# Kernel optimization log

Hardware: AMD Instinct MI355X
Metric: run time of the kernel (lower is better)

## Reference

```python
import jax, jax.numpy as jnp
import numpy as np


def setup_inputs() -> dict:
    key = jax.random.key(0)
    k1, k2 = jax.random.split(key)
    B, S, F = 8, 2048, 128
    feature = jax.random.normal(k1, (B, S, F), dtype=jnp.float32)
    noise = jax.random.normal(k2, (B, S, S), dtype=jnp.float32)
    return {"feature": feature, "noise": noise}


def reference(feature, noise):
    # stability: inverse variance over feat dim (torch.var is unbiased -> ddof=1)
    var = jnp.var(feature, axis=2, ddof=1, keepdims=True)          # [B, S, 1]
    stability = 1.0 / (var + 1e-6)
    stability = stability / jnp.max(stability)                      # global max normalize
    # scale per-row noise and softmax over keys (last dim)
    scaled = noise * stability                                      # [B, S, S]
    path = jax.nn.softmax(scaled, axis=-1)                          # [B, S, S]
    # weighted sum of frames
    return jnp.einsum('bij,bjf->bif', path, feature)                # [B, S, F]
```

## Files before the change

### kernel.cpp

```cpp
#include <hip/hip_runtime.h>
#include <hip/hip_bf16.h>

#define BATCH 8
#define SEQ   2048
#define FEATD 128
#define IBLK  32
#define JT    64
#define KSPLIT 2
#define KLEN  (SEQ / KSPLIT)
#define NJT   (KLEN / JT)

typedef __attribute__((ext_vector_type(8))) short short8;
typedef __attribute__((ext_vector_type(4))) float f32x4;

__device__ __forceinline__ unsigned short f2bf(float f) {
  unsigned int u = __float_as_uint(f);
  u += 0x7fffu + ((u >> 16) & 1u);
  return (unsigned short)(u >> 16);
}

__device__ __forceinline__ void gll16(const unsigned short* gsrc, unsigned short* lds) {
  __builtin_amdgcn_global_load_lds(
      (const __attribute__((address_space(1))) void*)gsrc,
      (__attribute__((address_space(3))) void*)lds, 16, 0, 0);
}

__global__ __launch_bounds__(256)
void prep_kernel(const float* __restrict__ feature,
                 float* __restrict__ stab,
                 unsigned int* __restrict__ gmax,
                 unsigned short* __restrict__ featT) {
  __shared__ float tile[32][133];
  __shared__ float wmax[4];
  int bid = blockIdx.x;
  int b   = bid >> 6;
  int j0  = (bid & 63) * 32;
  int t   = threadIdx.x;
  int r   = t >> 3;
  int seg = t & 7;

  const float* rp = feature + ((size_t)(b * SEQ + j0 + r)) * FEATD + seg * 16;
  float s = 0.0f, ss = 0.0f;
  #pragma unroll
  for (int k = 0; k < 4; k++) {
    float4 v = ((const float4*)rp)[k];
    tile[r][seg * 16 + k * 4 + 0] = v.x;
    tile[r][seg * 16 + k * 4 + 1] = v.y;
    tile[r][seg * 16 + k * 4 + 2] = v.z;
    tile[r][seg * 16 + k * 4 + 3] = v.w;
    s  += v.x + v.y + v.z + v.w;
    ss += v.x * v.x + v.y * v.y + v.z * v.z + v.w * v.w;
  }
  #pragma unroll
  for (int d = 1; d < 8; d <<= 1) {
    s  += __shfl_xor(s, d, 8);
    ss += __shfl_xor(ss, d, 8);
  }
  float st = 0.0f;
  if (seg == 0) {
    float var = (ss - s * s * (1.0f / 128.0f)) * (1.0f / 127.0f);
    st = 1.0f / (var + 1e-6f);
    stab[(size_t)b * SEQ + j0 + r] = st;
  }
  float m = st;
  #pragma unroll
  for (int d = 1; d < 64; d <<= 1) m = fmaxf(m, __shfl_xor(m, d, 64));
  if ((t & 63) == 0) wmax[t >> 6] = m;
  __syncthreads();
  if (t == 0) {
    float mm = fmaxf(fmaxf(wmax[0], wmax[1]), fmaxf(wmax[2], wmax[3]));
    atomicMax(gmax, __float_as_uint(mm));
  }
  int f  = t >> 1;
  int jh = t & 1;
  unsigned short obuf[16];
  #pragma unroll
  for (int jj = 0; jj < 16; jj++) obuf[jj] = f2bf(tile[jh * 16 + jj][f]);
  unsigned short* dst = featT + ((size_t)(b * FEATD + f)) * SEQ + j0 + jh * 16;
  *(uint4*)(dst)     = *(const uint4*)&obuf[0];
  *(uint4*)(dst + 8) = *(const uint4*)&obuf[8];
}

#define LOADN4(JTV, N0, N1, N2, N3) { \
    const float4* p_ = (const float4*)(nbase + (size_t)(JTV) * JT); \
    N0 = p_[0]; N1 = p_[1]; N2 = p_[8]; N3 = p_[9]; }

#define PROCB(N0, N1, N2, N3, PK0, PK1) { \
    float x_[16] = {N0.x, N0.y, N0.z, N0.w, N1.x, N1.y, N1.z, N1.w, \
                    N2.x, N2.y, N2.z, N2.w, N3.x, N3.y, N3.z, N3.w}; \
    _Pragma("unroll") \
    for (int k_ = 0; k_ < 8; k_++) { \
      float e_ = __expf(x_[k_] * sn); psum += e_; PK0[k_] = (short)f2bf(e_); } \
    _Pragma("unroll") \
    for (int k_ = 0; k_ < 8; k_++) { \
      float e_ = __expf(x_[8 + k_] * sn); psum += e_; PK1[k_] = (short)f2bf(e_); } }

#define GLLSLOT(JTV, SLOT) { \
    gll16(g0 + (size_t)(JTV) * JT, l0 + (SLOT) * (FEATD * JT)); \
    gll16(g1 + (size_t)(JTV) * JT, l1 + (SLOT) * (FEATD * JT)); \
    gll16(g2 + (size_t)(JTV) * JT, l2 + (SLOT) * (FEATD * JT)); \
    gll16(g3 + (size_t)(JTV) * JT, l3 + (SLOT) * (FEATD * JT)); }

#define DOMFMA(SLOT, PK0, PK1) { \
    _Pragma("unroll") \
    for (int fc = 0; fc < 4; fc++) { \
      const unsigned short* bp_ = &fT[SLOT][wf + fc * 16 + l15][0]; \
      short8 b0_ = *(const short8*)(bp_ + ((lg ^ sw7) << 3)); \
      short8 b1_ = *(const short8*)(bp_ + (((4 | lg) ^ sw7) << 3)); \
      acc[fc] = __builtin_amdgcn_mfma_f32_16x16x32_bf16(PK0, b0_, acc[fc], 0, 0, 0); \
      acc[fc] = __builtin_amdgcn_mfma_f32_16x16x32_bf16(PK1, b1_, acc[fc], 0, 0, 0); \
    } }

__global__ __launch_bounds__(256, 4)
void fused_kernel(const float* __restrict__ noise,
                  const unsigned short* __restrict__ featT,
                  const float* __restrict__ stab,
                  const unsigned int* __restrict__ gmaxp,
                  float* __restrict__ pout,
                  float* __restrict__ psums) {
  __shared__ unsigned short fT[2][FEATD][JT];

  int bid  = blockIdx.x;
  int b    = bid >> 7;
  int rest = bid & 127;
  int i0   = (rest >> 1) * IBLK;
  int ks   = rest & 1;
  int jb   = ks * KLEN;

  int t = threadIdx.x;
  int wv = t >> 6, lane = t & 63, l15 = lane & 15, lg = lane >> 4;
  int wi = (wv >> 1) * 16, wf = (wv & 1) * 64;
  int sw7 = l15 & 7;
  int row = i0 + wi + l15;

  float gmaxv = __uint_as_float(*gmaxp);
  float sn = stab[(size_t)b * SEQ + row] / gmaxv;

  const float* nbase = noise + ((size_t)b * SEQ + row) * SEQ + jb + lg * 8;

  unsigned short* lbase = &fT[0][0][0];
  const unsigned short* g0; const unsigned short* g1;
  const unsigned short* g2; const unsigned short* g3;
  unsigned short *l0, *l1, *l2, *l3;
  {
    int i0u = wv * 256 + lane;
    #define GSRC(M) (featT + ((size_t)(b * FEATD + ((i0u + 64*(M)) >> 3))) * SEQ + jb \
                     + ((((i0u + 64*(M)) & 7) ^ (((i0u + 64*(M)) >> 3) & 7)) * 8))
    g0 = GSRC(0); g1 = GSRC(1); g2 = GSRC(2); g3 = GSRC(3);
    #undef GSRC
    l0 = lbase + (wv * 256 + 0)   * 8;
    l1 = lbase + (wv * 256 + 64)  * 8;
    l2 = lbase + (wv * 256 + 128) * 8;
    l3 = lbase + (wv * 256 + 192) * 8;
  }

  f32x4 acc[4];
  #pragma unroll
  for (int k = 0; k < 4; k++) {
    f32x4 z = {0.0f, 0.0f, 0.0f, 0.0f};
    acc[k] = z;
  }
  float psum = 0.0f;

  float4 nA0, nA1, nA2, nA3, nB0, nB1, nB2, nB3;
  short8 pkA0, pkA1, pkB0, pkB1;

  GLLSLOT(0, 0);
  LOADN4(0, nA0, nA1, nA2, nA3);
  __syncthreads();

  for (int jt = 0; jt < NJT; jt += 2) {
    GLLSLOT(jt + 1, 1);
    LOADN4(jt + 1, nB0, nB1, nB2, nB3);
    PROCB(nA0, nA1, nA2, nA3, pkA0, pkA1);
    DOMFMA(0, pkA0, pkA1);
    __syncthreads();
    if (jt + 2 < NJT) {
      GLLSLOT(jt + 2, 0);
      LOADN4(jt + 2, nA0, nA1, nA2, nA3);
    }
    PROCB(nB0, nB1, nB2, nB3, pkB0, pkB1);
    DOMFMA(1, pkB0, pkB1);
    __syncthreads();
  }

  psum += __shfl_xor(psum, 16, 64);
  psum += __shfl_xor(psum, 32, 64);
  if ((wv & 1) == 0 && lg == 0) {
    psums[(size_t)ks * BATCH * SEQ + (size_t)b * SEQ + i0 + wi + l15] = psum;
  }

  float* orow = pout + (((size_t)(ks * BATCH + b)) * SEQ + i0 + wi) * FEATD + wf;
  #pragma unroll
  for (int v = 0; v < 4; v++) {
    int r = lg * 4 + v;
    #pragma unroll
    for (int fc = 0; fc < 4; fc++) {
      orow[(size_t)r * FEATD + fc * 16 + l15] = acc[fc][v];
    }
  }
}

__global__ __launch_bounds__(256)
void combine_kernel(const float* __restrict__ pout,
                    const float* __restrict__ psums,
                    float* __restrict__ out) {
  int e4 = blockIdx.x * 256 + threadIdx.x;
  int rowg = e4 >> 5;
  const float4* p0 = (const float4*)pout + e4;
  const float4* p1 = p0 + (size_t)BATCH * SEQ * FEATD / 4;
  float s = psums[rowg] + psums[BATCH * SEQ + rowg];
  float rinv = 1.0f / s;
  float4 a = *p0, c = *p1, o;
  o.x = (a.x + c.x) * rinv;
  o.y = (a.y + c.y) * rinv;
  o.z = (a.z + c.z) * rinv;
  o.w = (a.w + c.w) * rinv;
  ((float4*)out)[e4] = o;
}

extern "C" void kernel_launch(void* const* d_in, const int* in_sizes, int n_in,
                              void* d_out, int out_size, void* d_ws, size_t ws_size,
                              hipStream_t stream) {
  const float* feature = (const float*)d_in[0];
  const float* noise   = (const float*)d_in[1];
  float* out = (float*)d_out;

  float* stab           = (float*)d_ws;
  unsigned int* gmax    = (unsigned int*)((char*)d_ws + (64 << 10));
  unsigned short* featT = (unsigned short*)((char*)d_ws + (128 << 10));
  float* pout           = (float*)((char*)d_ws + (8 << 20));
  float* psums          = (float*)((char*)d_ws + (32 << 20));

  hipMemsetAsync(gmax, 0, sizeof(unsigned int), stream);
  prep_kernel<<<dim3(BATCH * SEQ / 32), dim3(256), 0, stream>>>(feature, stab, gmax, featT);
  fused_kernel<<<dim3(BATCH * (SEQ / IBLK) * KSPLIT), dim3(256), 0, stream>>>(
      noise, featT, stab, gmax, pout, psums);
  combine_kernel<<<dim3(BATCH * SEQ * FEATD / 4 / 256), dim3(256), 0, stream>>>(
      pout, psums, out);
}
```

Before: 228.6 us.

## Drop K-split and combine kernel; pipeline LDS loads with vmcnt barriers

The key-dimension split is removed, so each block walks the full sequence and normalises its output rows directly. This eliminates the partial-output buffers and the separate combine kernel. The main loop is also restructured: it uses a single barrier per tile with explicit s_waitcnt vmcnt, and it issues the next global-to-LDS load after the barrier so the loads overlap the MFMA work. The trade-off is half as many blocks (512 instead of 1024), which lowers parallelism and lengthens each block's serial loop. The hand-placed vmcnt counts must also stay correct for the data hazards on the LDS buffers.

```diff
diff --git a/kernel.cpp b/kernel.cpp
--- a/kernel.cpp
+++ b/kernel.cpp
@@ -6,9 +6,7 @@
 #define FEATD 128
 #define IBLK  32
 #define JT    64
-#define KSPLIT 2
-#define KLEN  (SEQ / KSPLIT)
-#define NJT   (KLEN / JT)
+#define NJT   (SEQ / JT)
 
 typedef __attribute__((ext_vector_type(8))) short short8;
 typedef __attribute__((ext_vector_type(4))) float f32x4;
@@ -111,21 +109,23 @@
       acc[fc] = __builtin_amdgcn_mfma_f32_16x16x32_bf16(PK1, b1_, acc[fc], 0, 0, 0); \
     } }
 
+#define VBAR(N) { \
+    asm volatile("s_waitcnt vmcnt(" #N ")" ::: "memory"); \
+    __builtin_amdgcn_s_barrier(); \
+    asm volatile("" ::: "memory"); \
+    __builtin_amdgcn_sched_barrier(0); }
+
 __global__ __launch_bounds__(256, 4)
 void fused_kernel(const float* __restrict__ noise,
                   const unsigned short* __restrict__ featT,
                   const float* __restrict__ stab,
                   const unsigned int* __restrict__ gmaxp,
-                  float* __restrict__ pout,
-                  float* __restrict__ psums) {
+                  float* __restrict__ out) {
   __shared__ unsigned short fT[2][FEATD][JT];
 
-  int bid  = blockIdx.x;
-  int b    = bid >> 7;
-  int rest = bid & 127;
-  int i0   = (rest >> 1) * IBLK;
-  int ks   = rest & 1;
-  int jb   = ks * KLEN;
+  int bid = blockIdx.x;
+  int b   = bid >> 6;
+  int i0  = (bid & 63) * IBLK;
 
   int t = threadIdx.x;
   int wv = t >> 6, lane = t & 63, l15 = lane & 15, lg = lane >> 4;
@@ -136,7 +136,7 @@
   float gmaxv = __uint_as_float(*gmaxp);
   float sn = stab[(size_t)b * SEQ + row] / gmaxv;
 
-  const float* nbase = noise + ((size_t)b * SEQ + row) * SEQ + jb + lg * 8;
+  const float* nbase = noise + ((size_t)b * SEQ + row) * SEQ + lg * 8;
 
   unsigned short* lbase = &fT[0][0][0];
   const unsigned short* g0; const unsigned short* g1;
@@ -144,7 +144,7 @@
   unsigned short *l0, *l1, *l2, *l3;
   {
     int i0u = wv * 256 + lane;
-    #define GSRC(M) (featT + ((size_t)(b * FEATD + ((i0u + 64*(M)) >> 3))) * SEQ + jb \
+    #define GSRC(M) (featT + ((size_t)(b * FEATD + ((i0u + 64*(M)) >> 3))) * SEQ \
                      + ((((i0u + 64*(M)) & 7) ^ (((i0u + 64*(M)) >> 3) & 7)) * 8))
     g0 = GSRC(0); g1 = GSRC(1); g2 = GSRC(2); g3 = GSRC(3);
     #undef GSRC
@@ -167,56 +167,43 @@
 
   GLLSLOT(0, 0);
   LOADN4(0, nA0, nA1, nA2, nA3);
-  __syncthreads();
-
-  for (int jt = 0; jt < NJT; jt += 2) {
-    GLLSLOT(jt + 1, 1);
+
+  for (int jt = 0; jt < NJT - 2; jt += 2) {
     LOADN4(jt + 1, nB0, nB1, nB2, nB3);
     PROCB(nA0, nA1, nA2, nA3, pkA0, pkA1);
+    VBAR(4);
+    GLLSLOT(jt + 1, 1);
     DOMFMA(0, pkA0, pkA1);
-    __syncthreads();
-    if (jt + 2 < NJT) {
-      GLLSLOT(jt + 2, 0);
-      LOADN4(jt + 2, nA0, nA1, nA2, nA3);
-    }
+    LOADN4(jt + 2, nA0, nA1, nA2, nA3);
     PROCB(nB0, nB1, nB2, nB3, pkB0, pkB1);
+    VBAR(4);
+    GLLSLOT(jt + 2, 0);
     DOMFMA(1, pkB0, pkB1);
-    __syncthreads();
-  }
+  }
+
+  LOADN4(NJT - 1, nB0, nB1, nB2, nB3);
+  PROCB(nA0, nA1, nA2, nA3, pkA0, pkA1);
+  VBAR(4);
+  GLLSLOT(NJT - 1, 1);
+  DOMFMA(0, pkA0, pkA1);
+  PROCB(nB0, nB1, nB2, nB3, pkB0, pkB1);
+  VBAR(0);
+  DOMFMA(1, pkB0, pkB1);
 
   psum += __shfl_xor(psum, 16, 64);
   psum += __shfl_xor(psum, 32, 64);
-  if ((wv & 1) == 0 && lg == 0) {
-    psums[(size_t)ks * BATCH * SEQ + (size_t)b * SEQ + i0 + wi + l15] = psum;
-  }
-
-  float* orow = pout + (((size_t)(ks * BATCH + b)) * SEQ + i0 + wi) * FEATD + wf;
+
+  float* orow = out + ((size_t)b * SEQ + i0 + wi) * FEATD + wf;
   #pragma unroll
   for (int v = 0; v < 4; v++) {
     int r = lg * 4 + v;
+    float rs = __shfl(psum, r, 64);
+    float rinv = 1.0f / rs;
     #pragma unroll
     for (int fc = 0; fc < 4; fc++) {
-      orow[(size_t)r * FEATD + fc * 16 + l15] = acc[fc][v];
+      orow[(size_t)r * FEATD + fc * 16 + l15] = acc[fc][v] * rinv;
     }
   }
-}
-
-__global__ __launch_bounds__(256)
-void combine_kernel(const float* __restrict__ pout,
-                    const float* __restrict__ psums,
-                    float* __restrict__ out) {
-  int e4 = blockIdx.x * 256 + threadIdx.x;
-  int rowg = e4 >> 5;
-  const float4* p0 = (const float4*)pout + e4;
-  const float4* p1 = p0 + (size_t)BATCH * SEQ * FEATD / 4;
-  float s = psums[rowg] + psums[BATCH * SEQ + rowg];
-  float rinv = 1.0f / s;
-  float4 a = *p0, c = *p1, o;
-  o.x = (a.x + c.x) * rinv;
-  o.y = (a.y + c.y) * rinv;
-  o.z = (a.z + c.z) * rinv;
-  o.w = (a.w + c.w) * rinv;
-  ((float4*)out)[e4] = o;
 }
 
 extern "C" void kernel_launch(void* const* d_in, const int* in_sizes, int n_in,
@@ -229,13 +216,8 @@
   float* stab           = (float*)d_ws;
   unsigned int* gmax    = (unsigned int*)((char*)d_ws + (64 << 10));
   unsigned short* featT = (unsigned short*)((char*)d_ws + (128 << 10));
-  float* pout           = (float*)((char*)d_ws + (8 << 20));
-  float* psums          = (float*)((char*)d_ws + (32 << 20));
 
   hipMemsetAsync(gmax, 0, sizeof(unsigned int), stream);
   prep_kernel<<<dim3(BATCH * SEQ / 32), dim3(256), 0, stream>>>(feature, stab, gmax, featT);
-  fused_kernel<<<dim3(BATCH * (SEQ / IBLK) * KSPLIT), dim3(256), 0, stream>>>(
-      noise, featT, stab, gmax, pout, psums);
-  combine_kernel<<<dim3(BATCH * SEQ * FEATD / 4 / 256), dim3(256), 0, stream>>>(
-      pout, psums, out);
-}
+  fused_kernel<<<dim3(BATCH * SEQ / IBLK), dim3(256), 0, stream>>>(noise, featT, stab, gmax, out);
+}
```

Result: no change. 226.0 us (-1.2%).
